# Kernel tuning notes

Hardware: AMD Instinct MI355X
Metric: run time of the kernel (lower is better)

Reference implementation:

```python
import jax, jax.numpy as jnp
import numpy as np

N_USER = 805   # herbs
N_ITEM = 390   # symptoms
N = 1195       # total nodes
D = 64         # embedding_dim (forced by final matmul)
E = 1_000_000
E_SUB = 500_000
B = 2048
BN_EPS = 1e-5


def _gcn(x, W, b, edge):
    # GCNConv_SH: message = Linear(x_j), aggr='mean', then tanh.
    # Linear commutes with mean (bias included when in-degree>0; isolated nodes -> 0),
    # so transform nodes once, then gather->segment-mean.
    h = x @ W.T + b                      # [N, D]
    src, dst = edge[0], edge[1]
    agg = jax.ops.segment_sum(h[src], dst, num_segments=N)          # [N, D]
    cnt = jax.ops.segment_sum(jnp.ones(edge.shape[1], x.dtype), dst, num_segments=N)
    mean = agg / jnp.maximum(cnt, 1.0)[:, None]   # isolated nodes stay 0 (PyG mean aggr)
    return jnp.tanh(mean)


def _two_layer(x, W1, b1, W2, b2, edge):
    return _gcn(_gcn(x, W1, b1, edge), W2, b2, edge)


def _norm(x, axis):
    # self.Norm(emb, count, n_dim): L2 normalize along n_dim (0 for user side, 1 for item side)
    return x / jnp.linalg.norm(x, axis=axis, keepdims=True)


def setup_inputs() -> dict:
    key = jax.random.key(0)
    ks = jax.random.split(key, 12)
    emb = jax.random.normal(ks[0], (N, D), jnp.float32)
    s = 1.0 / np.sqrt(D)
    W1 = jax.random.normal(ks[1], (D, D), jnp.float32) * s
    b1 = jnp.zeros((D,), jnp.float32)
    W2 = jax.random.normal(ks[2], (D, D), jnp.float32) * s
    b2 = jnp.zeros((D,), jnp.float32)
    mlp_W = jax.random.normal(ks[3], (64, D), jnp.float32) * s
    mlp_b = jnp.zeros((64,), jnp.float32)
    bn_gamma = jnp.ones((64,), jnp.float32)
    bn_beta = jnp.zeros((64,), jnp.float32)
    # multi-hot prescription; guarantee nonzero row sums for the mean-pool divide
    presc = (jax.random.uniform(ks[4], (B, N_ITEM)) < 0.05).astype(jnp.float32)
    presc = presc.at[:, 0].set(1.0)
    total_g = jax.random.randint(ks[5], (2, E), 0, N)
    sub_g1 = jax.random.randint(ks[6], (2, E_SUB), 0, N)
    sub_g2 = jax.random.randint(ks[7], (2, E_SUB), 0, N)
    edge_index_SH = jax.random.randint(ks[8], (2, 1000), 0, N)
    return {"edge_index_SH": edge_index_SH, "prescription": presc,
            "emb": emb, "W1": W1, "b1": b1, "W2": W2, "b2": b2,
            "mlp_W": mlp_W, "mlp_b": mlp_b, "bn_gamma": bn_gamma, "bn_beta": bn_beta,
            "total_g": total_g, "sub_g1": sub_g1, "sub_g2": sub_g2}


def reference(edge_index_SH, prescription, emb, W1, b1, W2, b2, mlp_W, mlp_b,
              bn_gamma, bn_beta, total_g, sub_g1, sub_g2):
    # edge_index_SH is accepted (forward signature) but unused, as in the source.
    x_SH1 = emb                                   # SH_embedding(arange(1195))
    x_SH6 = _two_layer(emb, W1, b1, W2, b2, total_g)   # two shared GCNConv_SH layers
    SH_g3 = _two_layer(emb, W1, b1, W2, b2, sub_g1)
    SH_g33 = _two_layer(emb, W1, b1, W2, b2, sub_g2)

    # ssl_layer_loss returns normalized previous (raw-embedding) views
    s_u = _norm(x_SH1[:N_USER], 0)   # [805, D]
    s_i = _norm(x_SH1[N_USER:], 1)   # [390, D]
    # sgl_loss returns normalized sub-graph-1 views
    n_u = _norm(SH_g3[:N_USER], 0)
    n_i = _norm(SH_g3[N_USER:], 1)
    # Same2Loss (reconstructed): fuse all contrastive views into final node reps
    c_u = 0.25 * (s_i + n_i + _norm(x_SH6[N_USER:], 1) + _norm(SH_g33[N_USER:], 1))  # [390, D]
    c_i = 0.25 * (s_u + n_u + _norm(x_SH6[:N_USER], 0) + _norm(SH_g33[:N_USER], 0))  # [805, D]

    e_synd = prescription @ c_u                           # [B, D]
    e_synd = e_synd / prescription.sum(axis=1, keepdims=True)
    h = e_synd @ mlp_W.T + mlp_b                          # [B, 64]
    mu = h.mean(axis=0)
    var = h.var(axis=0)                                   # biased, as torch BN training
    h = (h - mu) / jnp.sqrt(var + BN_EPS) * bn_gamma + bn_beta
    h = jax.nn.relu(h)
    pre = h @ c_i.T                                       # [B, 805]
    return pre
```

## Files before the change

### kernel.cpp

```cpp
#include <hip/hip_runtime.h>
#include <hip/hip_bf16.h>


#define NN    1195
#define NUSER 805
#define NITEM 390
#define DD    64
#define BB    2048
#define NPAD  1216
#define E_TOT 1000000
#define E_SUB 500000
#define MT    19
#define KT    8
#define CHUNK 3
#define LSTR  72
#define OUT2STRIDE (NN*DD)
#define CPG    299
#define P8W    152
#define FNT    13
#define KPAD   448
#define ENT    7

typedef unsigned int uint;
typedef unsigned short u16;
typedef unsigned char u8;
typedef __attribute__((ext_vector_type(8))) short short8;
typedef __attribute__((ext_vector_type(4))) float f32x4;

__device__ __forceinline__ float wsum(float v) {
#pragma unroll
    for (int m = 32; m > 0; m >>= 1) v += __shfl_xor(v, m, 64);
    return v;
}
__device__ __forceinline__ u16 f2b(float f) {
    uint u = __float_as_uint(f);
    return (u16)((u + 0x7FFFu + ((u >> 16) & 1u)) >> 16);
}
__device__ __forceinline__ float b2f16(u16 b) { return __uint_as_float(((uint)b) << 16); }
__device__ __forceinline__ void split4(const float* v, u16* hh, u16* ll) {
#pragma unroll
    for (int j = 0; j < 4; ++j) {
        u16 h = f2b(v[j]);
        hh[j] = h;
        ll[j] = f2b(v[j] - b2f16(h));
    }
}
__device__ __forceinline__ uint2 pack4(const u16* x) {
    uint2 o;
    o.x = (uint)x[0] | ((uint)x[1] << 16);
    o.y = (uint)x[2] | ((uint)x[3] << 16);
    return o;
}

#define CVT_EMB   0
#define CVT_W1    76480
#define CVT_B1    80576
#define CVT_W2    80640
#define CVT_B2    84736
#define CVT_MLPW  84800
#define CVT_MLPB  88896
#define CVT_GAMMA 88960
#define CVT_BETA  89024
#define CVT_TOTAL 89088

constexpr size_t alignUp64(size_t x) { return (x + 63) & ~size_t(63); }
constexpr size_t OFF_BNS  = 0;
constexpr size_t OFF_CNSS = 128;
constexpr size_t OFF_FLAG = 384;
constexpr size_t OFF_CVT  = 448;
constexpr size_t OFF_ABF  = alignUp64(OFF_CVT + CVT_TOTAL);
constexpr size_t OFF_RC   = alignUp64(OFF_ABF + (3ull * NN * NPAD) / 2);
constexpr size_t OFF_POOL = alignUp64(OFF_RC + 3ull * NPAD);


__global__ __launch_bounds__(1024, 8) void k_front(const void* presc, const void* emb,
        const void* p1, const void* p2, const void* p3, const void* p4,
        const void* p5, const void* p6, const void* p7, const void* p8, const void* p9,
        const int* __restrict__ tg, const int* __restrict__ s1, const int* __restrict__ s2,
        float* __restrict__ dst, float* __restrict__ cnss, float* __restrict__ bnsum,
        int* __restrict__ flag, uint* __restrict__ P8,
        int S0, int S1, int R, int rows, int HB) {
    extern __shared__ __align__(16) uint lds[];
    int b = blockIdx.x, t = threadIdx.x;
    int isbf = (((const u16*)presc)[0] == 0x3F80u) ? 1 : 0;
    if (b < HB) {
        int RS0 = R * S0, RS1 = R * S1;
        int g, p, r;
        if (b < RS0)            { g = 0; p = b % S0; r = b / S0; }
        else if (b < RS0 + RS1) { int b2 = b - RS0;        g = 1; p = b2 % S1; r = b2 / S1; }
        else                    { int b3 = b - RS0 - RS1;  g = 2; p = b3 % S1; r = b3 / S1; }
        int Sg = g ? S1 : S0;
        int cb = (g == 0) ? 0 : S0 + (g - 1) * S1;
        int r0 = r * rows;
        int nw4 = (rows * P8W) >> 2;
        {
            uint4* l4 = (uint4*)lds;
            for (int i = t; i < nw4; i += 1024) l4[i] = (uint4){0u, 0u, 0u, 0u};
        }
        __syncthreads();
        const int* eg = (g == 0) ? tg : (g == 1 ? s1 : s2);
        int Eg = (g == 0) ? E_TOT : E_SUB;
        int e0 = (int)(((long)p * Eg / Sg) & ~3L);
        int e1 = (p == Sg - 1) ? Eg : (int)(((long)(p + 1) * Eg / Sg) & ~3L);
        const int* srcp = eg;
        const int* dstp = eg + Eg;
        for (int i = e0 + t * 4; i < e1; i += 1024 * 4) {
            int4 d4 = *(const int4*)(dstp + i);
            int4 s4 = *(const int4*)(srcp + i);
            int rw;
            rw = d4.x - r0; if ((unsigned)rw < (unsigned)rows) atomicAdd(&lds[rw * P8W + (s4.x >> 3)], 1u << ((s4.x & 7) * 4));
            rw = d4.y - r0; if ((unsigned)rw < (unsigned)rows) atomicAdd(&lds[rw * P8W + (s4.y >> 3)], 1u << ((s4.y & 7) * 4));
            rw = d4.z - r0; if ((unsigned)rw < (unsigned)rows) atomicAdd(&lds[rw * P8W + (s4.z >> 3)], 1u << ((s4.z & 7) * 4));
            rw = d4.w - r0; if ((unsigned)rw < (unsigned)rows) atomicAdd(&lds[rw * P8W + (s4.w >> 3)], 1u << ((s4.w & 7) * 4));
        }
        __syncthreads();
        int rmax = rows; if (r0 + rmax > NN) rmax = NN - r0;
        uint* out = P8 + ((size_t)(cb + p) * NN + r0) * P8W;
        int n4 = (rmax * P8W) >> 2;
        const uint4* l4 = (const uint4*)lds;
        uint4* o4 = (uint4*)out;
        for (int i = t; i < n4; i += 1024) o4[i] = l4[i];
    } else if (b == HB) {
        if (t < 192) cnss[64 + t] = 0.0f;
        if (t < 128) bnsum[t] = 0.0f;
        int c = t & 63, chunk = t >> 6;
        float s = 0.0f;
        const u16* e16 = (const u16*)emb;
        const float* e32 = (const float*)emb;
        for (int r = chunk; r < NUSER; r += 16) {
            float v = isbf ? b2f16(e16[r * 64 + c]) : e32[r * 64 + c];
            s = fmaf(v, v, s);
        }
        float* sd = (float*)lds;
        sd[t] = s;
        __syncthreads();
        if (t < 64) {
            float tot = 0.0f;
#pragma unroll
            for (int j = 0; j < 16; ++j) tot += sd[j * 64 + t];
            cnss[t] = tot;
        }
    } else {
        int i = (b - HB - 1) * 1024 + t;
        if (i == 0) *flag = isbf;
        if (i < CVT_TOTAL) {
            const void* s2p; int o2;
            if      (i < CVT_W1)    { s2p = p1; o2 = i; }
            else if (i < CVT_B1)    { s2p = p2; o2 = i - CVT_W1; }
            else if (i < CVT_W2)    { s2p = p3; o2 = i - CVT_B1; }
            else if (i < CVT_B2)    { s2p = p4; o2 = i - CVT_W2; }
            else if (i < CVT_MLPW)  { s2p = p5; o2 = i - CVT_B2; }
            else if (i < CVT_MLPB)  { s2p = p6; o2 = i - CVT_MLPW; }
            else if (i < CVT_GAMMA) { s2p = p7; o2 = i - CVT_MLPB; }
            else if (i < CVT_BETA)  { s2p = p8; o2 = i - CVT_GAMMA; }
            else                    { s2p = p9; o2 = i - CVT_BETA; }
            dst[i] = isbf ? __bfloat162float(((const __hip_bfloat16*)s2p)[o2])
                          : ((const float*)s2p)[o2];
        }
    }
}

__device__ __forceinline__ void xf2_body(int g, int n0, int t,
        const float* xsrc, size_t xgstride,
        const float* part, const float* rcnt, int fromPart, int rowlim,
        const float* W, const float* bias,
        u16* Hhi, u16* Hlo, size_t hgstride, int ostride,
        u16* Ah, u16* Al, u16* Bh, u16* Bl, float* bs) {
    int w = t >> 6, l = t & 63;
    if (t < 64) bs[t] = bias ? bias[t] : 0.0f;
    int r = t >> 2, c0 = (t & 3) * 16;
    {
        const float* Wr = W + r * 64 + c0;
        float av[16];
#pragma unroll
        for (int j4 = 0; j4 < 4; ++j4) {
            float4 v = *(const float4*)(Wr + j4 * 4);
            av[j4*4+0] = v.x; av[j4*4+1] = v.y; av[j4*4+2] = v.z; av[j4*4+3] = v.w;
        }
#pragma unroll
        for (int j4 = 0; j4 < 4; ++j4) {
            u16 hh[4], ll[4];
            split4(av + j4*4, hh, ll);
            *(uint2*)(Ah + r * LSTR + c0 + j4*4) = pack4(hh);
            *(uint2*)(Al + r * LSTR + c0 + j4*4) = pack4(ll);
        }
    }
    {
        int node = n0 + r;
        float xr[16];
#pragma unroll
        for (int j = 0; j < 16; ++j) xr[j] = 0.0f;
        if (node < rowlim) {
            if (fromPart) {
#pragma unroll
                for (int k = 0; k < KT; ++k) {
                    const float* pp = part + (((size_t)k * 3 + g) * NPAD + node) * 64 + c0;
#pragma unroll
                    for (int j4 = 0; j4 < 4; ++j4) {
                        float4 v = *(const float4*)(pp + j4 * 4);
                        xr[j4*4+0] += v.x; xr[j4*4+1] += v.y;
                        xr[j4*4+2] += v.z; xr[j4*4+3] += v.w;
                    }
                }
                float rc = rcnt[g * NPAD + node];
#pragma unroll
                for (int j = 0; j < 16; ++j) xr[j] = tanhf(xr[j] * rc);
            } else {
                const float* Xr = xsrc + xgstride * g + (size_t)node * 64 + c0;
#pragma unroll
                for (int j4 = 0; j4 < 4; ++j4) {
                    float4 v = *(const float4*)(Xr + j4 * 4);
                    xr[j4*4+0] = v.x; xr[j4*4+1] = v.y;
                    xr[j4*4+2] = v.z; xr[j4*4+3] = v.w;
                }
            }
        }
#pragma unroll
        for (int j4 = 0; j4 < 4; ++j4) {
            u16 hh[4], ll[4];
            split4(xr + j4*4, hh, ll);
            *(uint2*)(Bh + r * LSTR + c0 + j4*4) = pack4(hh);
            *(uint2*)(Bl + r * LSTR + c0 + j4*4) = pack4(ll);
        }
    }
    __syncthreads();
    f32x4 acc[4];
#pragma unroll
    for (int p = 0; p < 4; ++p) acc[p] = (f32x4){0.f, 0.f, 0.f, 0.f};
    int mrow = w * 16 + (l & 15);
    int q8 = (l >> 4) * 8;
#pragma unroll
    for (int ks = 0; ks < 2; ++ks) {
        short8 ah = *(const short8*)(Ah + mrow * LSTR + ks * 32 + q8);
        short8 al = *(const short8*)(Al + mrow * LSTR + ks * 32 + q8);
#pragma unroll
        for (int p = 0; p < 4; ++p) {
            int nrow = p * 16 + (l & 15);
            short8 bh = *(const short8*)(Bh + nrow * LSTR + ks * 32 + q8);
            short8 bl = *(const short8*)(Bl + nrow * LSTR + ks * 32 + q8);
            acc[p] = __builtin_amdgcn_mfma_f32_16x16x32_bf16(ah, bh, acc[p], 0, 0, 0);
            acc[p] = __builtin_amdgcn_mfma_f32_16x16x32_bf16(ah, bl, acc[p], 0, 0, 0);
            acc[p] = __builtin_amdgcn_mfma_f32_16x16x32_bf16(al, bh, acc[p], 0, 0, 0);
        }
    }
    int q = l >> 4;
#pragma unroll
    for (int p = 0; p < 4; ++p) {
        int node = n0 + p * 16 + (l & 15);
#pragma unroll
        for (int rr2 = 0; rr2 < 4; ++rr2) {
            int d = w * 16 + q * 4 + rr2;
            float v = acc[p][rr2] + bs[d];
            u16 h = f2b(v);
            size_t o = hgstride * g + (size_t)d * ostride + node;
            Hhi[o] = h;
            Hlo[o] = f2b(v - b2f16(h));
        }
    }
}

__global__ __launch_bounds__(256) void k_xf2(const float* __restrict__ xsrc,
        size_t xgstride, const float* __restrict__ part, const float* __restrict__ rcnt,
        int fromPart, int ngb, int rowlim,
        const float* __restrict__ W, const float* __restrict__ bias,
        u16* __restrict__ Hhi, u16* __restrict__ Hlo, size_t hgstride, int ostride) {
    __shared__ u16 Ah[64 * LSTR], Al[64 * LSTR], Bh[64 * LSTR], Bl[64 * LSTR];
    __shared__ float bs[64];
    int b = blockIdx.x;
    xf2_body(b / ngb, (b % ngb) * 64, threadIdx.x, xsrc, xgstride, part, rcnt,
             fromPart, rowlim, W, bias, Hhi, Hlo, hgstride, ostride,
             Ah, Al, Bh, Bl, bs);
}

__global__ __launch_bounds__(256) void k_abf_xf1(const uint* __restrict__ P8,
        int S0, int S1,
        u16* __restrict__ Abf, float* __restrict__ rcnt,
        const float* __restrict__ embF, const float* __restrict__ W1,
        const float* __restrict__ b1, u16* __restrict__ H1hi, u16* __restrict__ H1lo) {
    __shared__ u16 Ah[64 * LSTR], Al[64 * LSTR], Bh[64 * LSTR], Bl[64 * LSTR];
    __shared__ float bs[64];
    __shared__ float ws4[4];
    int b = blockIdx.x, t = threadIdx.x;
    if (b < 3 * NN) {
        int g = b / NN, m = b % NN;
        int Sg = g ? S1 : S0;
        int cb = (g == 0) ? 0 : S0 + (g - 1) * S1;
        int w = t >> 6;
        float partial = 0.0f;
        if (t < P8W) {
            uint cnt[8] = {0, 0, 0, 0, 0, 0, 0, 0};
            for (int p = 0; p < Sg; ++p) {
                uint v = P8[((size_t)(cb + p) * NN + m) * P8W + t];
#pragma unroll
                for (int k = 0; k < 8; ++k) cnt[k] += (v >> (4 * k)) & 15u;
            }
            uint4 o;
            o.x = (uint)f2b((float)cnt[0]) | ((uint)f2b((float)cnt[1]) << 16);
            o.y = (uint)f2b((float)cnt[2]) | ((uint)f2b((float)cnt[3]) << 16);
            o.z = (uint)f2b((float)cnt[4]) | ((uint)f2b((float)cnt[5]) << 16);
            o.w = (uint)f2b((float)cnt[6]) | ((uint)f2b((float)cnt[7]) << 16);
            *(uint4*)(Abf + (size_t)b * NPAD + t * 8) = o;
#pragma unroll
            for (int k = 0; k < 8; ++k) partial += (float)cnt[k];
        }
        partial = wsum(partial);
        if ((t & 63) == 0) ws4[w] = partial;
        __syncthreads();
        if (t == 0)
            rcnt[g * NPAD + m] = 1.0f / fmaxf(ws4[0] + ws4[1] + ws4[2] + ws4[3], 1.0f);
    } else {
        int nt = b - 3 * NN;
        xf2_body(0, nt * 64, t, embF, 0, nullptr, nullptr, 0, NN, W1, b1,
                 H1hi, H1lo, 0, NPAD, Ah, Al, Bh, Bl, bs);
    }
}

__global__ __launch_bounds__(256) void k_aggp(const u16* __restrict__ Abf,
        const u16* __restrict__ Hhi, const u16* __restrict__ Hlo, size_t hstride,
        float* __restrict__ part) {
    int b = blockIdx.x;
    int kt = b & 7;
    int mt = (b >> 3) % MT;
    int g  = (b >> 3) / MT;
    int t = threadIdx.x, w = t >> 6, l = t & 63;
    __shared__ u16 As[64 * LSTR], Bh[64 * LSTR], Bl[64 * LSTR];
    f32x4 acc[4];
#pragma unroll
    for (int p = 0; p < 4; ++p) acc[p] = (f32x4){0.f, 0.f, 0.f, 0.f};
    int m0 = mt * 64;
    const u16* Ag = Abf + (size_t)g * NN * NPAD;
    const u16* Hg = Hhi + hstride * g;
    const u16* Lg = Hlo + hstride * g;
    int st0 = kt * CHUNK;
    int st1 = st0 + CHUNK; if (st1 > MT) st1 = MT;
    int rr = t >> 4, c4 = (t & 15) * 4;
    for (int st = st0; st < st1; ++st) {
        int s0 = st * 64;
        __syncthreads();
#pragma unroll
        for (int pass = 0; pass < 4; ++pass) {
            int r = pass * 16 + rr;
            uint2 av = {0u, 0u};
            if (m0 + r < NN) av = *(const uint2*)(Ag + (size_t)(m0 + r) * NPAD + s0 + c4);
            *(uint2*)(As + r * LSTR + c4) = av;
            *(uint2*)(Bh + r * LSTR + c4) = *(const uint2*)(Hg + (size_t)r * NPAD + s0 + c4);
            *(uint2*)(Bl + r * LSTR + c4) = *(const uint2*)(Lg + (size_t)r * NPAD + s0 + c4);
        }
        __syncthreads();
        int mrow = w * 16 + (l & 15);
        int q8 = (l >> 4) * 8;
#pragma unroll
        for (int ks = 0; ks < 2; ++ks) {
            short8 a = *(const short8*)(As + mrow * LSTR + ks * 32 + q8);
#pragma unroll
            for (int p = 0; p < 4; ++p) {
                int nrow = p * 16 + (l & 15);
                short8 bh = *(const short8*)(Bh + nrow * LSTR + ks * 32 + q8);
                short8 bl = *(const short8*)(Bl + nrow * LSTR + ks * 32 + q8);
                acc[p] = __builtin_amdgcn_mfma_f32_16x16x32_bf16(a, bh, acc[p], 0, 0, 0);
                acc[p] = __builtin_amdgcn_mfma_f32_16x16x32_bf16(a, bl, acc[p], 0, 0, 0);
            }
        }
    }
    int q = l >> 4;
#pragma unroll
    for (int p = 0; p < 4; ++p) {
        int n = p * 16 + (l & 15);
#pragma unroll
        for (int r = 0; r < 4; ++r) {
            int m = m0 + w * 16 + q * 4 + r;
            if (m < NN)
                part[(((size_t)kt * 3 + g) * NPAD + m) * 64 + n] = acc[p][r];
        }
    }
}

__global__ __launch_bounds__(256) void k_comb(const float* __restrict__ part,
        const float* __restrict__ rcnt, float* __restrict__ out, float* __restrict__ cnss) {
    int g = blockIdx.x / CPG, bi = blockIdx.x % CPG;
    int t = threadIdx.x;
    int idx = bi * 256 + t;
    int m = idx >> 6, n = idx & 63;
    bool valid = idx < NN * 64;
    float v = 0.0f;
    if (valid) {
        float s = 0.0f;
#pragma unroll
        for (int k = 0; k < KT; ++k)
            s += part[(((size_t)k * 3 + g) * NPAD + m) * 64 + n];
        v = tanhf(s * rcnt[g * NPAD + m]);
        out[(size_t)g * NN * 64 + idx] = v;
    }
    float x2 = (valid && m < NUSER) ? v * v : 0.0f;
    __shared__ float sd[256];
    sd[t] = x2;
    __syncthreads();
    if (t < 64) {
        float s = sd[t] + sd[t + 64] + sd[t + 128] + sd[t + 192];
        if (s != 0.0f) atomicAdd(&cnss[(g + 1) * 64 + t], s);
    }
}

__global__ void k_cuci(const float* __restrict__ embf, const float* __restrict__ out2,
                       const float* __restrict__ cnss, float* __restrict__ cu,
                       float* __restrict__ ci) {
    int b = blockIdx.x, l = threadIdx.x;
    if (b < 448) {
        if (b >= NITEM) { cu[(size_t)b * DD + l] = 0.0f; return; }
        int node = NUSER + b;
        const float* v0 = embf + (size_t)node * DD;
        const float* v1 = out2 + (size_t)node * DD;
        const float* v2 = out2 + OUT2STRIDE + (size_t)node * DD;
        const float* v3 = out2 + 2ull * OUT2STRIDE + (size_t)node * DD;
        float total = 0.0f;
        { float x = v0[l]; float ss = wsum(x * x); total += x / sqrtf(ss); }
        { float x = v1[l]; float ss = wsum(x * x); total += x / sqrtf(ss); }
        { float x = v2[l]; float ss = wsum(x * x); total += x / sqrtf(ss); }
        { float x = v3[l]; float ss = wsum(x * x); total += x / sqrtf(ss); }
        cu[(size_t)b * DD + l] = 0.25f * total;
    } else {
        int u = b - 448;
        size_t i = (size_t)u * DD + l;
        float s = embf[i] / sqrtf(cnss[l])
                + out2[i] / sqrtf(cnss[64 + l])
                + out2[OUT2STRIDE + i] / sqrtf(cnss[128 + l])
                + out2[2ull * OUT2STRIDE + i] / sqrtf(cnss[192 + l]);
        ci[i] = 0.25f * s;
    }
}

__global__ __launch_bounds__(256) void k_esynd(const void* __restrict__ presc,
        const u16* __restrict__ cwh, const u16* __restrict__ cwl,
        const float* __restrict__ mlpB, const int* __restrict__ flag,
        float* __restrict__ hpre, float* __restrict__ bnsum) {
    int m0 = blockIdx.x * 64;
    int t = threadIdx.x, w = t >> 6, l = t & 63;
    int isbf = *flag;
    const u16* pB = (const u16*)presc;
    const float* pF = (const float*)presc;
    __shared__ u16 As[64 * LSTR], Bh[64 * LSTR], Bl[64 * LSTR];
    __shared__ u16 Ones[16 * LSTR];
    __shared__ float bs[64];
    __shared__ float r1[4][64], r2[4][64];
    for (int i = t; i < 16 * LSTR; i += 256) Ones[i] = (i < 64) ? 0x3F80u : 0u;
    if (t < 64) bs[t] = mlpB[t];

    f32x4 acc[4], acc1;
#pragma unroll
    for (int p = 0; p < 4; ++p) acc[p] = (f32x4){0.f, 0.f, 0.f, 0.f};
    acc1 = (f32x4){0.f, 0.f, 0.f, 0.f};

    int rr = t >> 4, c4 = (t & 15) * 4;
    for (int st = 0; st < ENT; ++st) {
        int s0 = st * 64;
        __syncthreads();
#pragma unroll
        for (int pass = 0; pass < 4; ++pass) {
            int r = pass * 16 + rr;
            int m = m0 + r;
            int kb = s0 + c4;
            u16 a4[4];
            if (kb + 3 < NITEM) {
                if (isbf) {
                    const uint* p32 = (const uint*)pB + (((size_t)m * NITEM + kb) >> 1);
                    uint u0 = p32[0], u1 = p32[1];
                    a4[0] = (u16)u0; a4[1] = (u16)(u0 >> 16);
                    a4[2] = (u16)u1; a4[3] = (u16)(u1 >> 16);
                } else {
                    const float2* pf2 = (const float2*)(pF + (size_t)m * NITEM + kb);
                    float2 f0 = pf2[0], f1 = pf2[1];
                    a4[0] = f2b(f0.x); a4[1] = f2b(f0.y);
                    a4[2] = f2b(f1.x); a4[3] = f2b(f1.y);
                }
            } else {
#pragma unroll
                for (int j = 0; j < 4; ++j) {
                    int k = kb + j;
                    a4[j] = (k < NITEM)
                          ? (isbf ? pB[(size_t)m * NITEM + k] : f2b(pF[(size_t)m * NITEM + k]))
                          : (u16)0;
                }
            }
            uint2 o;
            o.x = (uint)a4[0] | ((uint)a4[1] << 16);
            o.y = (uint)a4[2] | ((uint)a4[3] << 16);
            *(uint2*)(As + r * LSTR + c4) = o;
            *(uint2*)(Bh + r * LSTR + c4) = *(const uint2*)(cwh + (size_t)r * KPAD + s0 + c4);
            *(uint2*)(Bl + r * LSTR + c4) = *(const uint2*)(cwl + (size_t)r * KPAD + s0 + c4);
        }
        __syncthreads();
        int mrow = w * 16 + (l & 15);
        int q8 = (l >> 4) * 8;
#pragma unroll
        for (int ks = 0; ks < 2; ++ks) {
            short8 a = *(const short8*)(As + mrow * LSTR + ks * 32 + q8);
            short8 on = *(const short8*)(Ones + (l & 15) * LSTR + ks * 32 + q8);
            acc1 = __builtin_amdgcn_mfma_f32_16x16x32_bf16(a, on, acc1, 0, 0, 0);
#pragma unroll
            for (int p = 0; p < 4; ++p) {
                int nrow = p * 16 + (l & 15);
                short8 bh = *(const short8*)(Bh + nrow * LSTR + ks * 32 + q8);
                short8 bl = *(const short8*)(Bl + nrow * LSTR + ks * 32 + q8);
                acc[p] = __builtin_amdgcn_mfma_f32_16x16x32_bf16(a, bh, acc[p], 0, 0, 0);
                acc[p] = __builtin_amdgcn_mfma_f32_16x16x32_bf16(a, bl, acc[p], 0, 0, 0);
            }
        }
    }
    float inv[4];
#pragma unroll
    for (int r = 0; r < 4; ++r)
        inv[r] = 1.0f / __shfl(acc1[r], l & 48, 64);
    int q = l >> 4;
#pragma unroll
    for (int p = 0; p < 4; ++p) {
        int col = p * 16 + (l & 15);
        float a = 0.0f, c = 0.0f;
#pragma unroll
        for (int r = 0; r < 4; ++r) {
            float hv = acc[p][r] * inv[r] + bs[col];
            hpre[(size_t)(m0 + w * 16 + q * 4 + r) * DD + col] = hv;
            a += hv; c = fmaf(hv, hv, c);
        }
        a += __shfl_xor(a, 16, 64); a += __shfl_xor(a, 32, 64);
        c += __shfl_xor(c, 16, 64); c += __shfl_xor(c, 32, 64);
        if (l < 16) { r1[w][col] = a; r2[w][col] = c; }
    }
    __syncthreads();
    if (t < 64) {
        atomicAdd(&bnsum[t],      r1[0][t] + r1[1][t] + r1[2][t] + r1[3][t]);
        atomicAdd(&bnsum[64 + t], r2[0][t] + r2[1][t] + r2[2][t] + r2[3][t]);
    }
}

__global__ __launch_bounds__(256) void k_final(const float* __restrict__ hpre,
        const float* __restrict__ bnsum, const float* __restrict__ gamma,
        const float* __restrict__ beta, const float* __restrict__ ci,
        void* __restrict__ out, const int* __restrict__ flag) {
    int b = blockIdx.x;
    int mt = b / FNT, nt = b % FNT;
    int m0 = mt * 64, n0 = nt * 64;
    int t = threadIdx.x, w = t >> 6, l = t & 63;
    __shared__ u16 Ah[64 * LSTR], Al[64 * LSTR], Bh[64 * LSTR], Bl[64 * LSTR];
    __shared__ float mn[64], rsg[64], bt[64];
    if (t < 64) {
        float mean = bnsum[t] * (1.0f / BB);
        float var = bnsum[64 + t] * (1.0f / BB) - mean * mean;
        mn[t] = mean;
        rsg[t] = gamma[t] / sqrtf(var + 1e-5f);
        bt[t] = beta[t];
    }
    __syncthreads();
    const float4* hp4 = (const float4*)(hpre + (size_t)m0 * 64);
    const float4* ci4 = (const float4*)ci;
#pragma unroll
    for (int k = 0; k < 4; ++k) {
        int i = t + k * 256;
        int r = i >> 4, c4 = (i & 15) * 4;
        float4 v = hp4[i];
        float vv[4] = {v.x, v.y, v.z, v.w};
        u16 hh[4], ll[4];
#pragma unroll
        for (int j = 0; j < 4; ++j) {
            int d = c4 + j;
            float x = fmaxf((vv[j] - mn[d]) * rsg[d] + bt[d], 0.0f);
            u16 hb = f2b(x);
            hh[j] = hb;
            ll[j] = f2b(x - b2f16(hb));
        }
        *(uint2*)(Ah + r * LSTR + c4) = pack4(hh);
        *(uint2*)(Al + r * LSTR + c4) = pack4(ll);
        int col = n0 + r;
        float4 cv = (col < NUSER) ? ci4[(size_t)col * 16 + (i & 15)]
                                  : (float4){0.f, 0.f, 0.f, 0.f};
        float cc[4] = {cv.x, cv.y, cv.z, cv.w};
        split4(cc, hh, ll);
        *(uint2*)(Bh + r * LSTR + c4) = pack4(hh);
        *(uint2*)(Bl + r * LSTR + c4) = pack4(ll);
    }
    __syncthreads();
    f32x4 acc[4];
#pragma unroll
    for (int p = 0; p < 4; ++p) acc[p] = (f32x4){0.f, 0.f, 0.f, 0.f};
    int mrow = w * 16 + (l & 15);
    int q8 = (l >> 4) * 8;
#pragma unroll
    for (int ks = 0; ks < 2; ++ks) {
        short8 ah = *(const short8*)(Ah + mrow * LSTR + ks * 32 + q8);
        short8 al = *(const short8*)(Al + mrow * LSTR + ks * 32 + q8);
#pragma unroll
        for (int p = 0; p < 4; ++p) {
            int nrow = p * 16 + (l & 15);
            short8 bh = *(const short8*)(Bh + nrow * LSTR + ks * 32 + q8);
            short8 bl = *(const short8*)(Bl + nrow * LSTR + ks * 32 + q8);
            acc[p] = __builtin_amdgcn_mfma_f32_16x16x32_bf16(ah, bh, acc[p], 0, 0, 0);
            acc[p] = __builtin_amdgcn_mfma_f32_16x16x32_bf16(ah, bl, acc[p], 0, 0, 0);
            acc[p] = __builtin_amdgcn_mfma_f32_16x16x32_bf16(al, bh, acc[p], 0, 0, 0);
        }
    }
    int isbf = *flag;
    int q = l >> 4;
#pragma unroll
    for (int p = 0; p < 4; ++p) {
        int col = n0 + p * 16 + (l & 15);
        if (col < NUSER) {
#pragma unroll
            for (int r = 0; r < 4; ++r) {
                int row = m0 + w * 16 + q * 4 + r;
                size_t o = (size_t)row * NUSER + col;
                if (isbf) ((__hip_bfloat16*)out)[o] = __float2bfloat16(acc[p][r]);
                else      ((float*)out)[o] = acc[p][r];
            }
        }
    }
}

extern "C" void kernel_launch(void* const* d_in, const int* in_sizes, int n_in,
                              void* d_out, int out_size, void* d_ws, size_t ws_size,
                              hipStream_t stream) {
    const void* presc = d_in[1];
    const void* emb   = d_in[2];
    const void* W1    = d_in[3];
    const void* b1    = d_in[4];
    const void* W2    = d_in[5];
    const void* b2    = d_in[6];
    const void* mlpW  = d_in[7];
    const void* mlpB  = d_in[8];
    const void* gamma = d_in[9];
    const void* beta  = d_in[10];
    const int* tg = (const int*)d_in[11];
    const int* s1 = (const int*)d_in[12];
    const int* s2 = (const int*)d_in[13];
    float* ws = (float*)d_ws;
    (void)in_sizes; (void)n_in; (void)out_size;

    float* bnsum = ws + OFF_BNS;
    float* cnss  = ws + OFF_CNSS;
    int*   flag  = (int*)(ws + OFF_FLAG);
    float* cvt   = ws + OFF_CVT;
    float* embF  = cvt + CVT_EMB;
    float* W1F   = cvt + CVT_W1;
    float* b1F   = cvt + CVT_B1;
    float* W2F   = cvt + CVT_W2;
    float* b2F   = cvt + CVT_B2;
    float* mlpWF = cvt + CVT_MLPW;
    float* mlpBF = cvt + CVT_MLPB;
    float* gamF  = cvt + CVT_GAMMA;
    float* betF  = cvt + CVT_BETA;
    u16*   Abf   = (u16*)(ws + OFF_ABF);
    float* rcnt  = ws + OFF_RC;
    uint*  P8    = (uint*)(ws + OFF_POOL);
    float* part  = ws + OFF_POOL;
    u16*   cwh   = (u16*)(ws + OFF_POOL);
    u16*   cwl   = cwh + 64ull * KPAD;

    static int g_rows = 0;
    if (g_rows == 0) {
        hipError_t e = hipFuncSetAttribute((const void*)k_front,
                hipFuncAttributeMaxDynamicSharedMemorySize, 128 * P8W * 4);
        g_rows = (e == hipSuccess) ? 128 : 96;
    }
    int rows = g_rows;
    int R = (NN + rows - 1) / rows;

    size_t cpw = (size_t)NN * P8W;
    size_t tailF = 760000;
    int SU = 1;
    if      ((OFF_POOL + 32 * cpw + tailF) * 4 <= ws_size) SU = 4;
    else if ((OFF_POOL + 16 * cpw + tailF) * 4 <= ws_size) SU = 2;
    int S0 = 4 * SU, S1 = 2 * SU;
    int copies = S0 + 2 * S1;

    size_t o = alignUp64(OFF_POOL + (size_t)copies * cpw);
    u16*   H1hi = (u16*)(ws + o);  u16* H1lo = H1hi + 64ull * NPAD;
    o = alignUp64(o + 64ull * NPAD);
    u16*   H2hi = (u16*)(ws + o);  u16* H2lo = H2hi + 3ull * 64 * NPAD;
    o = alignUp64(o + 3ull * 64 * NPAD);
    float* out2 = ws + o;          o = alignUp64(o + 3ull * NN * DD);
    float* cu   = ws + o;          o = alignUp64(o + 448ull * DD);
    float* ci   = ws + o;          o = alignUp64(o + (size_t)NUSER * DD);
    float* hpre = ws + o;

    int HB = R * copies;
    int CVTB = CVT_TOTAL / 1024;

    k_front<<<HB + 1 + CVTB, 1024, rows * P8W * 4, stream>>>(presc, emb,
        emb, W1, b1, W2, b2, mlpW, mlpB, gamma, beta,
        tg, s1, s2, cvt, cnss, bnsum, flag, P8, S0, S1, R, rows, HB);
    k_abf_xf1<<<3 * NN + MT, 256, 0, stream>>>(P8, S0, S1, Abf, rcnt,
        embF, W1F, b1F, H1hi, H1lo);
    k_aggp<<<3 * MT * KT, 256, 0, stream>>>(Abf, H1hi, H1lo, 0, part);
    k_xf2<<<3 * MT, 256, 0, stream>>>(nullptr, 0, part, rcnt, 1, MT, NN,
        W2F, b2F, H2hi, H2lo, 64ull * NPAD, NPAD);
    k_aggp<<<3 * MT * KT, 256, 0, stream>>>(Abf, H2hi, H2lo, 64ull * NPAD, part);
    k_comb<<<3 * CPG, 256, 0, stream>>>(part, rcnt, out2, cnss);
    k_cuci<<<448 + NUSER, 64, 0, stream>>>(embF, out2, cnss, cu, ci);
    k_xf2<<<ENT, 256, 0, stream>>>(cu, 0, nullptr, nullptr, 0, ENT, 448,
        mlpWF, nullptr, cwh, cwl, 0, KPAD);
    k_esynd<<<BB / 64, 256, 0, stream>>>(presc, cwh, cwl, mlpBF, flag, hpre, bnsum);
    k_final<<<(BB / 64) * FNT, 256, 0, stream>>>(hpre, bnsum, gamF, betF, ci, d_out, flag);
}
```

Measured before the change: 197.7 us.

## Fuse post-histogram stages into one persistent cooperative kernel with grid syncs

Replaces the chain of nine small kernel launches after the front kernel with a single cooperative persistent kernel. Each former kernel becomes a device body looped over virtual block indices, with grid-wide syncs between stages. Bodies are refactored to take shared memory from a common buffer and add leading __syncthreads for reuse. The aim is to remove per-launch overhead and idle gaps between small kernels, at the cost of grid-sync latency and reduced parallelism in large phases. A fallback path keeps the separate launches if cooperative launch fails.

```diff
diff --git a/kernel.cpp b/kernel.cpp
--- a/kernel.cpp
+++ b/kernel.cpp
@@ -1,5 +1,8 @@
 #include <hip/hip_runtime.h>
 #include <hip/hip_bf16.h>
+#include <hip/hip_cooperative_groups.h>
+
+namespace cg = cooperative_groups;
 
 
 #define NN    1195
@@ -20,6 +23,7 @@
 #define FNT    13
 #define KPAD   448
 #define ENT    7
+#define CUCIB  ((448 + NUSER + 3) / 4)
 
 typedef unsigned int uint;
 typedef unsigned short u16;
@@ -72,6 +76,7 @@
 constexpr size_t OFF_RC   = alignUp64(OFF_ABF + (3ull * NN * NPAD) / 2);
 constexpr size_t OFF_POOL = alignUp64(OFF_RC + 3ull * NPAD);
 
+#define SM_BYTES 37632
 
 __global__ __launch_bounds__(1024, 8) void k_front(const void* presc, const void* emb,
         const void* p1, const void* p2, const void* p3, const void* p4,
@@ -160,12 +165,45 @@
     }
 }
 
+
+__device__ __forceinline__ void merge_body(int b, int t, const uint* P8, int S0, int S1,
+        u16* Abf, float* rcnt, float* ws4) {
+    __syncthreads();
+    int g = b / NN, m = b % NN;
+    int Sg = g ? S1 : S0;
+    int cb = (g == 0) ? 0 : S0 + (g - 1) * S1;
+    int w = t >> 6;
+    float partial = 0.0f;
+    if (t < P8W) {
+        uint cnt[8] = {0, 0, 0, 0, 0, 0, 0, 0};
+        for (int p = 0; p < Sg; ++p) {
+            uint v = P8[((size_t)(cb + p) * NN + m) * P8W + t];
+#pragma unroll
+            for (int k = 0; k < 8; ++k) cnt[k] += (v >> (4 * k)) & 15u;
+        }
+        uint4 o;
+        o.x = (uint)f2b((float)cnt[0]) | ((uint)f2b((float)cnt[1]) << 16);
+        o.y = (uint)f2b((float)cnt[2]) | ((uint)f2b((float)cnt[3]) << 16);
+        o.z = (uint)f2b((float)cnt[4]) | ((uint)f2b((float)cnt[5]) << 16);
+        o.w = (uint)f2b((float)cnt[6]) | ((uint)f2b((float)cnt[7]) << 16);
+        *(uint4*)(Abf + (size_t)b * NPAD + t * 8) = o;
+#pragma unroll
+        for (int k = 0; k < 8; ++k) partial += (float)cnt[k];
+    }
+    partial = wsum(partial);
+    if ((t & 63) == 0) ws4[w] = partial;
+    __syncthreads();
+    if (t == 0)
+        rcnt[g * NPAD + m] = 1.0f / fmaxf(ws4[0] + ws4[1] + ws4[2] + ws4[3], 1.0f);
+}
+
 __device__ __forceinline__ void xf2_body(int g, int n0, int t,
         const float* xsrc, size_t xgstride,
         const float* part, const float* rcnt, int fromPart, int rowlim,
         const float* W, const float* bias,
         u16* Hhi, u16* Hlo, size_t hgstride, int ostride,
         u16* Ah, u16* Al, u16* Bh, u16* Bl, float* bs) {
+    __syncthreads();
     int w = t >> 6, l = t & 63;
     if (t < 64) bs[t] = bias ? bias[t] : 0.0f;
     int r = t >> 2, c0 = (t & 3) * 16;
@@ -259,71 +297,13 @@
     }
 }
 
-__global__ __launch_bounds__(256) void k_xf2(const float* __restrict__ xsrc,
-        size_t xgstride, const float* __restrict__ part, const float* __restrict__ rcnt,
-        int fromPart, int ngb, int rowlim,
-        const float* __restrict__ W, const float* __restrict__ bias,
-        u16* __restrict__ Hhi, u16* __restrict__ Hlo, size_t hgstride, int ostride) {
-    __shared__ u16 Ah[64 * LSTR], Al[64 * LSTR], Bh[64 * LSTR], Bl[64 * LSTR];
-    __shared__ float bs[64];
-    int b = blockIdx.x;
-    xf2_body(b / ngb, (b % ngb) * 64, threadIdx.x, xsrc, xgstride, part, rcnt,
-             fromPart, rowlim, W, bias, Hhi, Hlo, hgstride, ostride,
-             Ah, Al, Bh, Bl, bs);
-}
-
-__global__ __launch_bounds__(256) void k_abf_xf1(const uint* __restrict__ P8,
-        int S0, int S1,
-        u16* __restrict__ Abf, float* __restrict__ rcnt,
-        const float* __restrict__ embF, const float* __restrict__ W1,
-        const float* __restrict__ b1, u16* __restrict__ H1hi, u16* __restrict__ H1lo) {
-    __shared__ u16 Ah[64 * LSTR], Al[64 * LSTR], Bh[64 * LSTR], Bl[64 * LSTR];
-    __shared__ float bs[64];
-    __shared__ float ws4[4];
-    int b = blockIdx.x, t = threadIdx.x;
-    if (b < 3 * NN) {
-        int g = b / NN, m = b % NN;
-        int Sg = g ? S1 : S0;
-        int cb = (g == 0) ? 0 : S0 + (g - 1) * S1;
-        int w = t >> 6;
-        float partial = 0.0f;
-        if (t < P8W) {
-            uint cnt[8] = {0, 0, 0, 0, 0, 0, 0, 0};
-            for (int p = 0; p < Sg; ++p) {
-                uint v = P8[((size_t)(cb + p) * NN + m) * P8W + t];
-#pragma unroll
-                for (int k = 0; k < 8; ++k) cnt[k] += (v >> (4 * k)) & 15u;
-            }
-            uint4 o;
-            o.x = (uint)f2b((float)cnt[0]) | ((uint)f2b((float)cnt[1]) << 16);
-            o.y = (uint)f2b((float)cnt[2]) | ((uint)f2b((float)cnt[3]) << 16);
-            o.z = (uint)f2b((float)cnt[4]) | ((uint)f2b((float)cnt[5]) << 16);
-            o.w = (uint)f2b((float)cnt[6]) | ((uint)f2b((float)cnt[7]) << 16);
-            *(uint4*)(Abf + (size_t)b * NPAD + t * 8) = o;
-#pragma unroll
-            for (int k = 0; k < 8; ++k) partial += (float)cnt[k];
-        }
-        partial = wsum(partial);
-        if ((t & 63) == 0) ws4[w] = partial;
-        __syncthreads();
-        if (t == 0)
-            rcnt[g * NPAD + m] = 1.0f / fmaxf(ws4[0] + ws4[1] + ws4[2] + ws4[3], 1.0f);
-    } else {
-        int nt = b - 3 * NN;
-        xf2_body(0, nt * 64, t, embF, 0, nullptr, nullptr, 0, NN, W1, b1,
-                 H1hi, H1lo, 0, NPAD, Ah, Al, Bh, Bl, bs);
-    }
-}
-
-__global__ __launch_bounds__(256) void k_aggp(const u16* __restrict__ Abf,
-        const u16* __restrict__ Hhi, const u16* __restrict__ Hlo, size_t hstride,
-        float* __restrict__ part) {
-    int b = blockIdx.x;
+__device__ __forceinline__ void aggp_body(int b, int t, const u16* Abf,
+        const u16* Hhi, const u16* Hlo, size_t hstride, float* part,
+        u16* As, u16* Bh, u16* Bl) {
     int kt = b & 7;
     int mt = (b >> 3) % MT;
     int g  = (b >> 3) / MT;
-    int t = threadIdx.x, w = t >> 6, l = t & 63;
-    __shared__ u16 As[64 * LSTR], Bh[64 * LSTR], Bl[64 * LSTR];
+    int w = t >> 6, l = t & 63;
     f32x4 acc[4];
 #pragma unroll
     for (int p = 0; p < 4; ++p) acc[p] = (f32x4){0.f, 0.f, 0.f, 0.f};
@@ -375,10 +355,10 @@
     }
 }
 
-__global__ __launch_bounds__(256) void k_comb(const float* __restrict__ part,
-        const float* __restrict__ rcnt, float* __restrict__ out, float* __restrict__ cnss) {
-    int g = blockIdx.x / CPG, bi = blockIdx.x % CPG;
-    int t = threadIdx.x;
+__device__ __forceinline__ void comb_body(int b, int t, const float* part,
+        const float* rcnt, float* out, float* cnss, float* sd) {
+    __syncthreads();
+    int g = b / CPG, bi = b % CPG;
     int idx = bi * 256 + t;
     int m = idx >> 6, n = idx & 63;
     bool valid = idx < NN * 64;
@@ -392,7 +372,6 @@
         out[(size_t)g * NN * 64 + idx] = v;
     }
     float x2 = (valid && m < NUSER) ? v * v : 0.0f;
-    __shared__ float sd[256];
     sd[t] = x2;
     __syncthreads();
     if (t < 64) {
@@ -401,10 +380,11 @@
     }
 }
 
-__global__ void k_cuci(const float* __restrict__ embf, const float* __restrict__ out2,
-                       const float* __restrict__ cnss, float* __restrict__ cu,
-                       float* __restrict__ ci) {
-    int b = blockIdx.x, l = threadIdx.x;
+__device__ __forceinline__ void cuci_body(int vb, int t, const float* embf,
+        const float* out2, const float* cnss, float* cu, float* ci) {
+    int b = vb * 4 + (t >> 6);
+    int l = t & 63;
+    if (b >= 448 + NUSER) return;
     if (b < 448) {
         if (b >= NITEM) { cu[(size_t)b * DD + l] = 0.0f; return; }
         int node = NUSER + b;
@@ -429,19 +409,22 @@
     }
 }
 
-__global__ __launch_bounds__(256) void k_esynd(const void* __restrict__ presc,
-        const u16* __restrict__ cwh, const u16* __restrict__ cwl,
-        const float* __restrict__ mlpB, const int* __restrict__ flag,
-        float* __restrict__ hpre, float* __restrict__ bnsum) {
-    int m0 = blockIdx.x * 64;
-    int t = threadIdx.x, w = t >> 6, l = t & 63;
+__device__ __forceinline__ void esynd_body(int bb, int t, const void* presc,
+        const u16* cwh, const u16* cwl, const float* mlpB, const int* flag,
+        float* hpre, float* bnsum, u8* smem) {
+    u16* As   = (u16*)smem;
+    u16* Bh   = (u16*)(smem + 9216);
+    u16* Bl   = (u16*)(smem + 18432);
+    u16* Ones = (u16*)(smem + 27648);
+    float* bs = (float*)(smem + 29952);
+    float* r1 = (float*)(smem + 30208);
+    float* r2 = (float*)(smem + 31232);
+    __syncthreads();
+    int m0 = bb * 64;
+    int w = t >> 6, l = t & 63;
     int isbf = *flag;
     const u16* pB = (const u16*)presc;
     const float* pF = (const float*)presc;
-    __shared__ u16 As[64 * LSTR], Bh[64 * LSTR], Bl[64 * LSTR];
-    __shared__ u16 Ones[16 * LSTR];
-    __shared__ float bs[64];
-    __shared__ float r1[4][64], r2[4][64];
     for (int i = t; i < 16 * LSTR; i += 256) Ones[i] = (i < 64) ? 0x3F80u : 0u;
     if (t < 64) bs[t] = mlpB[t];
 
@@ -523,25 +506,29 @@
         }
         a += __shfl_xor(a, 16, 64); a += __shfl_xor(a, 32, 64);
         c += __shfl_xor(c, 16, 64); c += __shfl_xor(c, 32, 64);
-        if (l < 16) { r1[w][col] = a; r2[w][col] = c; }
+        if (l < 16) { r1[w * 64 + col] = a; r2[w * 64 + col] = c; }
     }
     __syncthreads();
     if (t < 64) {
-        atomicAdd(&bnsum[t],      r1[0][t] + r1[1][t] + r1[2][t] + r1[3][t]);
-        atomicAdd(&bnsum[64 + t], r2[0][t] + r2[1][t] + r2[2][t] + r2[3][t]);
-    }
-}
-
-__global__ __launch_bounds__(256) void k_final(const float* __restrict__ hpre,
-        const float* __restrict__ bnsum, const float* __restrict__ gamma,
-        const float* __restrict__ beta, const float* __restrict__ ci,
-        void* __restrict__ out, const int* __restrict__ flag) {
-    int b = blockIdx.x;
-    int mt = b / FNT, nt = b % FNT;
+        atomicAdd(&bnsum[t],      r1[t] + r1[64 + t] + r1[128 + t] + r1[192 + t]);
+        atomicAdd(&bnsum[64 + t], r2[t] + r2[64 + t] + r2[128 + t] + r2[192 + t]);
+    }
+}
+
+__device__ __forceinline__ void final_body(int vb, int t, const float* hpre,
+        const float* bnsum, const float* gamma, const float* beta, const float* ci,
+        void* out, const int* flag, u8* smem) {
+    u16* Ah = (u16*)smem;
+    u16* Al = (u16*)(smem + 9216);
+    u16* Bh = (u16*)(smem + 18432);
+    u16* Bl = (u16*)(smem + 27648);
+    float* mn  = (float*)(smem + 36864);
+    float* rsg = (float*)(smem + 37120);
+    float* bt  = (float*)(smem + 37376);
+    __syncthreads();
+    int mt = vb / FNT, nt = vb % FNT;
     int m0 = mt * 64, n0 = nt * 64;
-    int t = threadIdx.x, w = t >> 6, l = t & 63;
-    __shared__ u16 Ah[64 * LSTR], Al[64 * LSTR], Bh[64 * LSTR], Bl[64 * LSTR];
-    __shared__ float mn[64], rsg[64], bt[64];
+    int w = t >> 6, l = t & 63;
     if (t < 64) {
         float mean = bnsum[t] * (1.0f / BB);
         float var = bnsum[64 + t] * (1.0f / BB) - mean * mean;
@@ -612,6 +599,127 @@
             }
         }
     }
+}
+
+struct MegaArgs {
+    const uint* P8; int S0; int S1;
+    u16* Abf; float* rcnt;
+    const float* embF; const float* W1F; const float* b1F;
+    u16* H1hi; u16* H1lo;
+    const float* W2F; const float* b2F;
+    u16* H2hi; u16* H2lo;
+    float* part;
+    float* out2; float* cnss;
+    float* cu; float* ci;
+    u16* cwh; u16* cwl;
+    const float* mlpWF; const float* mlpBF;
+    const int* flag; const void* presc;
+    float* hpre; float* bnsum;
+    const float* gamF; const float* betF;
+    void* out;
+};
+
+__global__ __launch_bounds__(256, 4) void k_mega(MegaArgs a) {
+    cg::grid_group gg = cg::this_grid();
+    __shared__ __align__(16) u8 smem[SM_BYTES];
+    int t = threadIdx.x;
+    int G = gridDim.x;
+    u16* Ah = (u16*)smem;
+    u16* Al = (u16*)(smem + 9216);
+    u16* Bh = (u16*)(smem + 18432);
+    u16* Bl = (u16*)(smem + 27648);
+    float* fep = (float*)(smem + 36864);
+
+    for (int vb = blockIdx.x; vb < 3 * NN + MT; vb += G) {
+        if (vb < 3 * NN)
+            merge_body(vb, t, a.P8, a.S0, a.S1, a.Abf, a.rcnt, (float*)smem);
+        else
+            xf2_body(0, (vb - 3 * NN) * 64, t, a.embF, 0, nullptr, nullptr, 0, NN,
+                     a.W1F, a.b1F, a.H1hi, a.H1lo, 0, NPAD, Ah, Al, Bh, Bl, fep);
+    }
+    gg.sync();
+    for (int vb = blockIdx.x; vb < 3 * MT * KT; vb += G)
+        aggp_body(vb, t, a.Abf, a.H1hi, a.H1lo, 0, a.part, Ah, Bh, Bl);
+    gg.sync();
+    for (int vb = blockIdx.x; vb < 3 * MT; vb += G)
+        xf2_body(vb / MT, (vb % MT) * 64, t, nullptr, 0, a.part, a.rcnt, 1, NN,
+                 a.W2F, a.b2F, a.H2hi, a.H2lo, 64ull * NPAD, NPAD, Ah, Al, Bh, Bl, fep);
+    gg.sync();
+    for (int vb = blockIdx.x; vb < 3 * MT * KT; vb += G)
+        aggp_body(vb, t, a.Abf, a.H2hi, a.H2lo, 64ull * NPAD, a.part, Ah, Bh, Bl);
+    gg.sync();
+    for (int vb = blockIdx.x; vb < 3 * CPG; vb += G)
+        comb_body(vb, t, a.part, a.rcnt, a.out2, a.cnss, (float*)smem);
+    gg.sync();
+    for (int vb = blockIdx.x; vb < CUCIB; vb += G)
+        cuci_body(vb, t, a.embF, a.out2, a.cnss, a.cu, a.ci);
+    gg.sync();
+    for (int vb = blockIdx.x; vb < ENT; vb += G)
+        xf2_body(0, vb * 64, t, a.cu, 0, nullptr, nullptr, 0, 448,
+                 a.mlpWF, nullptr, a.cwh, a.cwl, 0, KPAD, Ah, Al, Bh, Bl, fep);
+    gg.sync();
+    for (int vb = blockIdx.x; vb < BB / 64; vb += G)
+        esynd_body(vb, t, a.presc, a.cwh, a.cwl, a.mlpBF, a.flag, a.hpre, a.bnsum, smem);
+    gg.sync();
+    for (int vb = blockIdx.x; vb < (BB / 64) * FNT; vb += G)
+        final_body(vb, t, a.hpre, a.bnsum, a.gamF, a.betF, a.ci, a.out, a.flag, smem);
+}
+
+__global__ __launch_bounds__(256) void k_abf_xf1(const uint* __restrict__ P8,
+        int S0, int S1, u16* __restrict__ Abf, float* __restrict__ rcnt,
+        const float* __restrict__ embF, const float* __restrict__ W1,
+        const float* __restrict__ b1, u16* __restrict__ H1hi, u16* __restrict__ H1lo) {
+    __shared__ __align__(16) u8 smem[SM_BYTES];
+    int b = blockIdx.x, t = threadIdx.x;
+    if (b < 3 * NN)
+        merge_body(b, t, P8, S0, S1, Abf, rcnt, (float*)smem);
+    else
+        xf2_body(0, (b - 3 * NN) * 64, t, embF, 0, nullptr, nullptr, 0, NN, W1, b1,
+                 H1hi, H1lo, 0, NPAD, (u16*)smem, (u16*)(smem + 9216),
+                 (u16*)(smem + 18432), (u16*)(smem + 27648), (float*)(smem + 36864));
+}
+__global__ __launch_bounds__(256) void k_xf2(const float* __restrict__ xsrc,
+        size_t xgstride, const float* __restrict__ part, const float* __restrict__ rcnt,
+        int fromPart, int ngb, int rowlim,
+        const float* __restrict__ W, const float* __restrict__ bias,
+        u16* __restrict__ Hhi, u16* __restrict__ Hlo, size_t hgstride, int ostride) {
+    __shared__ __align__(16) u8 smem[SM_BYTES];
+    int b = blockIdx.x;
+    xf2_body(b / ngb, (b % ngb) * 64, threadIdx.x, xsrc, xgstride, part, rcnt,
+             fromPart, rowlim, W, bias, Hhi, Hlo, hgstride, ostride,
+             (u16*)smem, (u16*)(smem + 9216), (u16*)(smem + 18432),
+             (u16*)(smem + 27648), (float*)(smem + 36864));
+}
+__global__ __launch_bounds__(256) void k_aggp(const u16* __restrict__ Abf,
+        const u16* __restrict__ Hhi, const u16* __restrict__ Hlo, size_t hstride,
+        float* __restrict__ part) {
+    __shared__ __align__(16) u8 smem[27648];
+    aggp_body(blockIdx.x, threadIdx.x, Abf, Hhi, Hlo, hstride, part,
+              (u16*)smem, (u16*)(smem + 9216), (u16*)(smem + 18432));
+}
+__global__ __launch_bounds__(256) void k_comb(const float* __restrict__ part,
+        const float* __restrict__ rcnt, float* __restrict__ out, float* __restrict__ cnss) {
+    __shared__ float sd[256];
+    comb_body(blockIdx.x, threadIdx.x, part, rcnt, out, cnss, sd);
+}
+__global__ __launch_bounds__(256) void k_cuci(const float* __restrict__ embf,
+        const float* __restrict__ out2, const float* __restrict__ cnss,
+        float* __restrict__ cu, float* __restrict__ ci) {
+    cuci_body(blockIdx.x, threadIdx.x, embf, out2, cnss, cu, ci);
+}
+__global__ __launch_bounds__(256) void k_esynd(const void* __restrict__ presc,
+        const u16* __restrict__ cwh, const u16* __restrict__ cwl,
+        const float* __restrict__ mlpB, const int* __restrict__ flag,
+        float* __restrict__ hpre, float* __restrict__ bnsum) {
+    __shared__ __align__(16) u8 smem[32256];
+    esynd_body(blockIdx.x, threadIdx.x, presc, cwh, cwl, mlpB, flag, hpre, bnsum, smem);
+}
+__global__ __launch_bounds__(256) void k_final(const float* __restrict__ hpre,
+        const float* __restrict__ bnsum, const float* __restrict__ gamma,
+        const float* __restrict__ beta, const float* __restrict__ ci,
+        void* __restrict__ out, const int* __restrict__ flag) {
+    __shared__ __align__(16) u8 smem[SM_BYTES];
+    final_body(blockIdx.x, threadIdx.x, hpre, bnsum, gamma, beta, ci, out, flag, smem);
 }
 
 extern "C" void kernel_launch(void* const* d_in, const int* in_sizes, int n_in,
@@ -654,14 +762,24 @@
     u16*   cwl   = cwh + 64ull * KPAD;
 
     static int g_rows = 0;
+    static int g_grid = 0;
+    static int g_coop = -1;
     if (g_rows == 0) {
         hipError_t e = hipFuncSetAttribute((const void*)k_front,
                 hipFuncAttributeMaxDynamicSharedMemorySize, 128 * P8W * 4);
         g_rows = (e == hipSuccess) ? 128 : 96;
     }
+    if (g_grid == 0) {
+        int nb = 0;
+        hipError_t e = hipOccupancyMaxActiveBlocksPerMultiprocessor(&nb, k_mega, 256, 0);
+        if (e != hipSuccess || nb < 1) nb = 1;
+        long g = (long)nb * 256;
+        if (g > 1024) g = 1024;
+        g_grid = (int)g;
+    }
+
     int rows = g_rows;
     int R = (NN + rows - 1) / rows;
-
     size_t cpw = (size_t)NN * P8W;
     size_t tailF = 760000;
     int SU = 1;
@@ -681,21 +799,50 @@
     float* hpre = ws + o;
 
     int HB = R * copies;
-    int CVTB = CVT_TOTAL / 1024;
+    int CVTB = (CVT_TOTAL + 1023) / 1024;
 
     k_front<<<HB + 1 + CVTB, 1024, rows * P8W * 4, stream>>>(presc, emb,
         emb, W1, b1, W2, b2, mlpW, mlpB, gamma, beta,
         tg, s1, s2, cvt, cnss, bnsum, flag, P8, S0, S1, R, rows, HB);
-    k_abf_xf1<<<3 * NN + MT, 256, 0, stream>>>(P8, S0, S1, Abf, rcnt,
-        embF, W1F, b1F, H1hi, H1lo);
-    k_aggp<<<3 * MT * KT, 256, 0, stream>>>(Abf, H1hi, H1lo, 0, part);
-    k_xf2<<<3 * MT, 256, 0, stream>>>(nullptr, 0, part, rcnt, 1, MT, NN,
-        W2F, b2F, H2hi, H2lo, 64ull * NPAD, NPAD);
-    k_aggp<<<3 * MT * KT, 256, 0, stream>>>(Abf, H2hi, H2lo, 64ull * NPAD, part);
-    k_comb<<<3 * CPG, 256, 0, stream>>>(part, rcnt, out2, cnss);
-    k_cuci<<<448 + NUSER, 64, 0, stream>>>(embF, out2, cnss, cu, ci);
-    k_xf2<<<ENT, 256, 0, stream>>>(cu, 0, nullptr, nullptr, 0, ENT, 448,
-        mlpWF, nullptr, cwh, cwl, 0, KPAD);
-    k_esynd<<<BB / 64, 256, 0, stream>>>(presc, cwh, cwl, mlpBF, flag, hpre, bnsum);
-    k_final<<<(BB / 64) * FNT, 256, 0, stream>>>(hpre, bnsum, gamF, betF, ci, d_out, flag);
-}
+
+    MegaArgs ma;
+    ma.P8 = P8; ma.S0 = S0; ma.S1 = S1;
+    ma.Abf = Abf; ma.rcnt = rcnt;
+    ma.embF = embF; ma.W1F = W1F; ma.b1F = b1F;
+    ma.H1hi = H1hi; ma.H1lo = H1lo;
+    ma.W2F = W2F; ma.b2F = b2F;
+    ma.H2hi = H2hi; ma.H2lo = H2lo;
+    ma.part = part;
+    ma.out2 = out2; ma.cnss = cnss;
+    ma.cu = cu; ma.ci = ci;
+    ma.cwh = cwh; ma.cwl = cwl;
+    ma.mlpWF = mlpWF; ma.mlpBF = mlpBF;
+    ma.flag = flag; ma.presc = presc;
+    ma.hpre = hpre; ma.bnsum = bnsum;
+    ma.gamF = gamF; ma.betF = betF;
+    ma.out = d_out;
+
+    bool done = false;
+    if (g_coop != 0) {
+        void* kargs[] = { (void*)&ma };
+        hipError_t e = hipLaunchCooperativeKernel(k_mega, dim3(g_grid), dim3(256),
+                                                  kargs, 0, stream);
+        if (e == hipSuccess) { done = true; g_coop = 1; }
+        else { g_coop = 0; (void)hipGetLastError(); }
+    }
+    if (!done) {
+        k_abf_xf1<<<3 * NN + MT, 256, 0, stream>>>(P8, S0, S1, Abf, rcnt,
+            embF, W1F, b1F, H1hi, H1lo);
+        k_aggp<<<3 * MT * KT, 256, 0, stream>>>(Abf, H1hi, H1lo, 0, part);
+        k_xf2<<<3 * MT, 256, 0, stream>>>(nullptr, 0, part, rcnt, 1, MT, NN,
+            W2F, b2F, H2hi, H2lo, 64ull * NPAD, NPAD);
+        k_aggp<<<3 * MT * KT, 256, 0, stream>>>(Abf, H2hi, H2lo, 64ull * NPAD, part);
+        k_comb<<<3 * CPG, 256, 0, stream>>>(part, rcnt, out2, cnss);
+        k_cuci<<<CUCIB, 256, 0, stream>>>(embF, out2, cnss, cu, ci);
+        k_xf2<<<ENT, 256, 0, stream>>>(cu, 0, nullptr, nullptr, 0, ENT, 448,
+            mlpWF, nullptr, cwh, cwl, 0, KPAD);
+        k_esynd<<<BB / 64, 256, 0, stream>>>(presc, cwh, cwl, mlpBF, flag, hpre, bnsum);
+        k_final<<<(BB / 64) * FNT, 256, 0, stream>>>(hpre, bnsum, gamF, betF, ci,
+            d_out, flag);
+    }
+}
```

Measured after the change: 684.8 us. 246% more time.
